# Kernel optimization log

Hardware: AMD Instinct MI355X
Metric: run time of the kernel (lower is better)

The kernel has to match this reference:

```python
import jax, jax.numpy as jnp
import numpy as np

B, IN, H = 4096, 1024, 1024


def setup_inputs() -> dict:
    key = jax.random.key(0)
    ks = jax.random.split(key, 20)
    s_in = 1.0 / np.sqrt(IN)
    s_h = 1.0 / np.sqrt(H)
    def lin(kw, kb, fan_in, scale):
        W = jax.random.uniform(kw, (H, fan_in), jnp.float32, -scale, scale)
        b = jax.random.uniform(kb, (H,), jnp.float32, -scale, scale)
        return W, b
    Wxf, bxf = lin(ks[0], ks[1], IN, s_in)
    Whf, bhf = lin(ks[2], ks[3], H, s_h)
    Wxi, bxi = lin(ks[4], ks[5], IN, s_in)
    Whi, bhi = lin(ks[6], ks[7], H, s_h)
    Wxo, bxo = lin(ks[8], ks[9], IN, s_in)
    Who, bho = lin(ks[10], ks[11], H, s_h)
    Wxc, bxc = lin(ks[12], ks[13], IN, s_in)
    Whc, bhc = lin(ks[14], ks[15], H, s_h)
    x = jax.random.normal(ks[16], (B, IN), jnp.float32)
    c = jax.random.normal(ks[17], (B, H), jnp.float32)
    h = jax.random.normal(ks[18], (B, H), jnp.float32)
    return dict(x=x, c=c, h=h,
                Wxf=Wxf, bxf=bxf, Whf=Whf, bhf=bhf,
                Wxi=Wxi, bxi=bxi, Whi=Whi, bhi=bhi,
                Wxo=Wxo, bxo=bxo, Who=Who, bho=bho,
                Wxc=Wxc, bxc=bxc, Whc=Whc, bhc=bhc)


def reference(x, c, h,
              Wxf, bxf, Whf, bhf,
              Wxi, bxi, Whi, bhi,
              Wxo, bxo, Who, bho,
              Wxc, bxc, Whc, bhc):
    # Fuse the 8 small GEMMs into two batched GEMMs: x @ Wx^T and h @ Wh^T
    # with gate outputs concatenated along the hidden dim [f, i, o, c~].
    Wx = jnp.concatenate([Wxf, Wxi, Wxo, Wxc], axis=0)   # [4H, IN]
    Wh = jnp.concatenate([Whf, Whi, Who, Whc], axis=0)   # [4H, H]
    bx = jnp.concatenate([bxf, bxi, bxo, bxc], axis=0)   # [4H]
    bh = jnp.concatenate([bhf, bhi, bho, bhc], axis=0)   # [4H]
    gates = x @ Wx.T + h @ Wh.T + (bx + bh)              # [B, 4H]
    hs = Wxf.shape[0]
    f = jax.nn.sigmoid(gates[:, 0 * hs:1 * hs])
    i = jax.nn.sigmoid(gates[:, 1 * hs:2 * hs])
    o = jax.nn.sigmoid(gates[:, 2 * hs:3 * hs])
    ctil = jnp.tanh(gates[:, 3 * hs:4 * hs])
    ct = f * c + ctil * i
    ht = jnp.tanh(ct) * o
    return (ct, ht)
```

## Files before the change

### kernel.cpp

```cpp
#include <hip/hip_runtime.h>
#include <hip/hip_bf16.h>
#include <stdint.h>

typedef __hip_bfloat16 bf16;
typedef __attribute__((ext_vector_type(8))) short short8;
typedef __attribute__((ext_vector_type(4))) float floatx4;

#define AS1(p) ((const __attribute__((address_space(1))) void*)(p))
#define AS3(p) ((__attribute__((address_space(3))) void*)(p))

#define M_DIM 4096
#define H_DIM 1024
#define MEG   (1u << 20)
#define LDS_BUF 24576

__device__ __forceinline__ unsigned short f2bf(float f) {
    uint32_t u = __float_as_uint(f);
    uint32_t r = (u + 0x7FFFu + ((u >> 16) & 1u)) >> 16;
    return (unsigned short)r;
}

__device__ __forceinline__ float fast_sigmoid(float v) {
    return 1.0f / (1.0f + __expf(-v));
}
__device__ __forceinline__ float fast_tanh(float v) {
    return 2.0f / (1.0f + __expf(-2.0f * v)) - 1.0f;
}

__global__ __launch_bounds__(256)
void convert_to_bf16(const float* __restrict__ x, const float* __restrict__ h,
                     const float* Wxf, const float* Wxi, const float* Wxo, const float* Wxc,
                     const float* Whf, const float* Whi, const float* Who, const float* Whc,
                     unsigned short* __restrict__ ws)
{
    const uint32_t idx0 = blockIdx.x * 2048u + threadIdx.x * 8u;
    const uint32_t t = blockIdx.x >> 9;
    const float* src;
    uint32_t off;
    if (t < 4u)      { src = x; off = idx0; }
    else if (t < 8u) { src = h; off = idx0 - (4u << 20); }
    else {
        const uint32_t g = t - 8u;
        src = (g == 0) ? Wxf : (g == 1) ? Wxi : (g == 2) ? Wxo : (g == 3) ? Wxc
            : (g == 4) ? Whf : (g == 5) ? Whi : (g == 6) ? Who : Whc;
        off = idx0 & (MEG - 1u);
    }
    const float4 v0 = *(const float4*)(src + off);
    const float4 v1 = *(const float4*)(src + off + 4);
    short8 pk;
    pk[0] = (short)f2bf(v0.x); pk[1] = (short)f2bf(v0.y);
    pk[2] = (short)f2bf(v0.z); pk[3] = (short)f2bf(v0.w);
    pk[4] = (short)f2bf(v1.x); pk[5] = (short)f2bf(v1.y);
    pk[6] = (short)f2bf(v1.z); pk[7] = (short)f2bf(v1.w);
    *(short8*)(ws + idx0) = pk;
}

__global__ __launch_bounds__(256, 2)
void lstm_fused_kernel(const unsigned short* __restrict__ ws,
                       const float* __restrict__ c,
                       const float* __restrict__ bxf, const float* __restrict__ bhf,
                       const float* __restrict__ bxi, const float* __restrict__ bhi,
                       const float* __restrict__ bxo, const float* __restrict__ bho,
                       const float* __restrict__ bxc, const float* __restrict__ bhc,
                       float* __restrict__ out)
{
    __shared__ __align__(16) char lds[2 * LDS_BUF];

    const int tid  = threadIdx.x;
    const int w    = tid >> 6;
    const int lane = tid & 63;

    const int bm0 = blockIdx.x * 128;
    const int bn0 = blockIdx.y * 64;

    const uint32_t cg = (((uint32_t)lane & 3u) ^ (((uint32_t)lane >> 3) & 3u)) * 8u;
    const unsigned short* srcP0[6];
    const unsigned short* srcP1[6];
    uint32_t goff[6];
    uint32_t loff[6];
#pragma unroll
    for (int i = 0; i < 6; ++i) {
        const int ch = w * 6 + i;
        if (ch < 8) {
            const int row = bm0 + ch * 16 + (lane >> 2);
            srcP0[i] = ws;
            srcP1[i] = ws + (4u << 20);
            goff[i] = (uint32_t)row * 1024u + cg;
            loff[i] = (uint32_t)ch * 1024u;
        } else {
            const int b = ch - 8;
            const int g = b >> 2;
            const int n = bn0 + (b & 3) * 16 + (lane >> 2);
            srcP0[i] = ws + (8u << 20)  + (uint32_t)g * MEG;
            srcP1[i] = ws + (12u << 20) + (uint32_t)g * MEG;
            goff[i] = (uint32_t)n * 1024u + cg;
            loff[i] = 8192u + (uint32_t)b * 1024u;
        }
    }

    const int wrow  = (w & 1) * 64;
    const int wcol  = (w >> 1) * 32;
    const int lrc   = lane & 15;
    const int lquad = lane >> 4;

    const uint32_t kslot = (((uint32_t)lquad ^ (((uint32_t)lrc >> 1) & 3u))) * 8u;

    uint32_t aoff[4];
#pragma unroll
    for (int mt = 0; mt < 4; ++mt)
        aoff[mt] = (uint32_t)((wrow + mt * 16 + lrc) * 32) + kslot;
    uint32_t boff[4][2];
#pragma unroll
    for (int g = 0; g < 4; ++g)
#pragma unroll
        for (int nt = 0; nt < 2; ++nt)
            boff[g][nt] = (uint32_t)(g * 2048 + (wcol + nt * 16 + lrc) * 32) + kslot;

    floatx4 acc[4][4][2];
#pragma unroll
    for (int g = 0; g < 4; ++g)
#pragma unroll
        for (int mt = 0; mt < 4; ++mt)
#pragma unroll
            for (int nt = 0; nt < 2; ++nt)
                acc[g][mt][nt] = (floatx4){0.f, 0.f, 0.f, 0.f};

    auto issue_loads = [&](int kt) {
        const int phase = kt >> 5;
        const uint32_t k0 = (uint32_t)(kt & 31) * 32u;
        const uint32_t bb = (uint32_t)(kt & 1) * LDS_BUF;
#pragma unroll
        for (int i = 0; i < 6; ++i) {
            const unsigned short* src = phase ? srcP1[i] : srcP0[i];
            __builtin_amdgcn_global_load_lds(AS1(src + goff[i] + k0),
                                             AS3(lds + bb + loff[i]), 16, 0, 0);
        }
    };
    auto compute = [&](int kt) {
        const char* base = lds + (uint32_t)(kt & 1) * LDS_BUF;
        const bf16* lA = (const bf16*)base;
        const bf16* lB = (const bf16*)(base + 8192);
        short8 afr[4];
#pragma unroll
        for (int mt = 0; mt < 4; ++mt)
            afr[mt] = *(const short8*)(lA + aoff[mt]);
#pragma unroll
        for (int g = 0; g < 4; ++g) {
#pragma unroll
            for (int nt = 0; nt < 2; ++nt) {
                const short8 bfr = *(const short8*)(lB + boff[g][nt]);
#pragma unroll
                for (int mt = 0; mt < 4; ++mt)
                    acc[g][mt][nt] = __builtin_amdgcn_mfma_f32_16x16x32_bf16(
                        afr[mt], bfr, acc[g][mt][nt], 0, 0, 0);
            }
        }
    };

    issue_loads(0);
    asm volatile("s_waitcnt vmcnt(0)\ns_barrier" ::: "memory");

    for (int kt = 0; kt < 63; ++kt) {
        issue_loads(kt + 1);
        asm volatile("s_waitcnt vmcnt(6)\ns_barrier" ::: "memory");
        compute(kt);
        asm volatile("s_waitcnt lgkmcnt(0)\ns_barrier" ::: "memory");
    }
    asm volatile("s_waitcnt vmcnt(0)\ns_barrier" ::: "memory");
    compute(63);

    float* out_ct = out;
    float* out_ht = out + (size_t)M_DIM * H_DIM;
#pragma unroll
    for (int nt = 0; nt < 2; ++nt) {
        const int col = bn0 + wcol + nt * 16 + lrc;
        const float bf_ = bxf[col] + bhf[col];
        const float bi_ = bxi[col] + bhi[col];
        const float bo_ = bxo[col] + bho[col];
        const float bc_ = bxc[col] + bhc[col];
#pragma unroll
        for (int mt = 0; mt < 4; ++mt) {
#pragma unroll
            for (int r = 0; r < 4; ++r) {
                const int row = bm0 + wrow + mt * 16 + lquad * 4 + r;
                const float gf = acc[0][mt][nt][r] + bf_;
                const float gi = acc[1][mt][nt][r] + bi_;
                const float go = acc[2][mt][nt][r] + bo_;
                const float gc = acc[3][mt][nt][r] + bc_;
                const float f    = fast_sigmoid(gf);
                const float ii   = fast_sigmoid(gi);
                const float o    = fast_sigmoid(go);
                const float ctil = fast_tanh(gc);
                const float cv   = c[(size_t)row * H_DIM + col];
                const float ctn  = f * cv + ctil * ii;
                const float htn  = fast_tanh(ctn) * o;
                out_ct[(size_t)row * H_DIM + col] = ctn;
                out_ht[(size_t)row * H_DIM + col] = htn;
            }
        }
    }
}

extern "C" void kernel_launch(void* const* d_in, const int* in_sizes, int n_in,
                              void* d_out, int out_size, void* d_ws, size_t ws_size,
                              hipStream_t stream) {
    (void)in_sizes; (void)n_in; (void)out_size; (void)ws_size;
    const float* x   = (const float*)d_in[0];
    const float* c   = (const float*)d_in[1];
    const float* h   = (const float*)d_in[2];
    const float* Wxf = (const float*)d_in[3];  const float* bxf = (const float*)d_in[4];
    const float* Whf = (const float*)d_in[5];  const float* bhf = (const float*)d_in[6];
    const float* Wxi = (const float*)d_in[7];  const float* bxi = (const float*)d_in[8];
    const float* Whi = (const float*)d_in[9];  const float* bhi = (const float*)d_in[10];
    const float* Wxo = (const float*)d_in[11]; const float* bxo = (const float*)d_in[12];
    const float* Who = (const float*)d_in[13]; const float* bho = (const float*)d_in[14];
    const float* Wxc = (const float*)d_in[15]; const float* bxc = (const float*)d_in[16];
    const float* Whc = (const float*)d_in[17]; const float* bhc = (const float*)d_in[18];
    float* out = (float*)d_out;
    unsigned short* ws = (unsigned short*)d_ws;

    convert_to_bf16<<<8192, 256, 0, stream>>>(x, h,
        Wxf, Wxi, Wxo, Wxc, Whf, Whi, Who, Whc, ws);

    dim3 grid(M_DIM / 128, H_DIM / 64);
    lstm_fused_kernel<<<grid, 256, 0, stream>>>(ws, c,
        bxf, bhf, bxi, bhi, bxo, bho, bxc, bhc, out);
}
```

Measured before the change: 222.9 us.

## Use triple-buffered LDS pipeline and remap block IDs for L2 locality

Grows the LDS staging from two buffers to three so loads for k-tile kt+2 are issued while tile kt is computed. This removes one barrier per iteration and gives global loads more time to land. The 2D grid becomes a 1D grid of 512 blocks, with a block-ID remap that spreads neighbouring blocks across N tiles that share the same M rows, aiming for better L2 reuse. The extra LDS (72KB per block) may lower occupancy against the launch_bounds target of 2 blocks per CU.

```diff
diff --git a/kernel.cpp b/kernel.cpp
--- a/kernel.cpp
+++ b/kernel.cpp
@@ -64,14 +64,17 @@
                        const float* __restrict__ bxc, const float* __restrict__ bhc,
                        float* __restrict__ out)
 {
-    __shared__ __align__(16) char lds[2 * LDS_BUF];
+    __shared__ __align__(16) char lds[3 * LDS_BUF];
 
     const int tid  = threadIdx.x;
     const int w    = tid >> 6;
     const int lane = tid & 63;
 
-    const int bm0 = blockIdx.x * 128;
-    const int bn0 = blockIdx.y * 64;
+    const int bid = blockIdx.x;
+    const int mx  = bid >> 4;
+    const int ny  = ((bid & 7) << 1) | ((bid >> 3) & 1);
+    const int bm0 = mx * 128;
+    const int bn0 = ny * 64;
 
     const uint32_t cg = (((uint32_t)lane & 3u) ^ (((uint32_t)lane >> 3) & 3u)) * 8u;
     const unsigned short* srcP0[6];
@@ -125,10 +128,10 @@
             for (int nt = 0; nt < 2; ++nt)
                 acc[g][mt][nt] = (floatx4){0.f, 0.f, 0.f, 0.f};
 
-    auto issue_loads = [&](int kt) {
+    auto issue_loads = [&](int kt, uint32_t stage) {
         const int phase = kt >> 5;
         const uint32_t k0 = (uint32_t)(kt & 31) * 32u;
-        const uint32_t bb = (uint32_t)(kt & 1) * LDS_BUF;
+        const uint32_t bb = stage * LDS_BUF;
 #pragma unroll
         for (int i = 0; i < 6; ++i) {
             const unsigned short* src = phase ? srcP1[i] : srcP0[i];
@@ -136,8 +139,8 @@
                                              AS3(lds + bb + loff[i]), 16, 0, 0);
         }
     };
-    auto compute = [&](int kt) {
-        const char* base = lds + (uint32_t)(kt & 1) * LDS_BUF;
+    auto compute = [&](uint32_t stage) {
+        const char* base = lds + stage * LDS_BUF;
         const bf16* lA = (const bf16*)base;
         const bf16* lB = (const bf16*)(base + 8192);
         short8 afr[4];
@@ -157,17 +160,23 @@
         }
     };
 
-    issue_loads(0);
+    issue_loads(0, 0);
+    issue_loads(1, 1);
+
+    uint32_t s_comp = 0;
+    uint32_t s_load = 2;
+    for (int kt = 0; kt < 62; ++kt) {
+        asm volatile("s_waitcnt vmcnt(6)\ns_barrier" ::: "memory");
+        issue_loads(kt + 2, s_load);
+        compute(s_comp);
+        s_comp = (s_comp == 2) ? 0 : s_comp + 1;
+        s_load = (s_load == 2) ? 0 : s_load + 1;
+    }
+    asm volatile("s_waitcnt vmcnt(6)\ns_barrier" ::: "memory");
+    compute(s_comp);
+    s_comp = (s_comp == 2) ? 0 : s_comp + 1;
     asm volatile("s_waitcnt vmcnt(0)\ns_barrier" ::: "memory");
-
-    for (int kt = 0; kt < 63; ++kt) {
-        issue_loads(kt + 1);
-        asm volatile("s_waitcnt vmcnt(6)\ns_barrier" ::: "memory");
-        compute(kt);
-        asm volatile("s_waitcnt lgkmcnt(0)\ns_barrier" ::: "memory");
-    }
-    asm volatile("s_waitcnt vmcnt(0)\ns_barrier" ::: "memory");
-    compute(63);
+    compute(s_comp);
 
     float* out_ct = out;
     float* out_ht = out + (size_t)M_DIM * H_DIM;
@@ -222,7 +231,6 @@
     convert_to_bf16<<<8192, 256, 0, stream>>>(x, h,
         Wxf, Wxi, Wxo, Wxc, Whf, Whi, Who, Whc, ws);
 
-    dim3 grid(M_DIM / 128, H_DIM / 64);
-    lstm_fused_kernel<<<grid, 256, 0, stream>>>(ws, c,
+    lstm_fused_kernel<<<512, 256, 0, stream>>>(ws, c,
         bxf, bhf, bxi, bhi, bxo, bho, bxc, bhc, out);
 }
```

Result: no change. 224.3 us (+0.6%).
